# Kernel optimization log

Measured on AMD Instinct MI355X. Metric: run time of the kernel, lower is better.

## Reference

```python
import jax, jax.numpy as jnp
import numpy as np

N = 50000      # nodes
E = 400000     # edges (before self loops)
F_IN = 128     # num_features
HID = 64       # hidden_dim
HEADS = 4
G = 64         # number of graphs in batch
NCLS = 2
NEG = 0.2      # leaky relu negative slope
BN_EPS = 1e-5


def setup_inputs() -> dict:
    key = jax.random.key(0)
    ks = jax.random.split(key, 32)
    rn = lambda k, shape, s=0.05: jax.random.normal(k, shape, jnp.float32) * s
    inp = {}
    inp["x"] = jax.random.normal(ks[0], (N, F_IN), jnp.float32)
    inp["edge_index"] = jax.random.randint(ks[1], (2, E), 0, N, dtype=jnp.int32)
    inp["batch"] = jnp.sort(jax.random.randint(ks[2], (N,), 0, G, dtype=jnp.int32))
    # layer 0 GATConv (concat=True) + pre projection
    inp["conv0_W"] = rn(ks[3], (F_IN, HEADS * HID))
    inp["conv0_att_src"] = rn(ks[4], (HEADS, HID))
    inp["conv0_att_dst"] = rn(ks[5], (HEADS, HID))
    inp["conv0_bias"] = jnp.zeros((HEADS * HID,), jnp.float32)
    inp["pre0_W"] = rn(ks[6], (HEADS * HID, HID))
    inp["pre0_b"] = jnp.zeros((HID,), jnp.float32)
    # layers 1..2 GATConv (concat=False), stacked
    inp["convs_W"] = rn(ks[7], (2, HID, HEADS * HID))
    inp["convs_att_src"] = rn(ks[8], (2, HEADS, HID))
    inp["convs_att_dst"] = rn(ks[9], (2, HEADS, HID))
    inp["convs_bias"] = jnp.zeros((2, HID), jnp.float32)
    # batch norms (eval mode: running stats)
    inp["bn_gamma"] = jnp.ones((3, HID), jnp.float32)
    inp["bn_beta"] = jnp.zeros((3, HID), jnp.float32)
    inp["bn_mean"] = rn(ks[10], (3, HID), 0.1)
    inp["bn_var"] = jax.random.uniform(ks[11], (3, HID), jnp.float32) + 0.5
    # JK projection, attention pooling, classifier
    inp["jump_W"] = rn(ks[12], (3 * HID, HID))
    inp["jump_b"] = jnp.zeros((HID,), jnp.float32)
    inp["att_W"] = rn(ks[13], (HID, 1))
    inp["att_b"] = jnp.zeros((1,), jnp.float32)
    inp["cls_W1"] = rn(ks[14], (HID, HID // 2))
    inp["cls_b1"] = jnp.zeros((HID // 2,), jnp.float32)
    inp["cls_W2"] = rn(ks[15], (HID // 2, NCLS))
    inp["cls_b2"] = jnp.zeros((NCLS,), jnp.float32)
    return inp


def _segment_softmax(logits, seg, num_segments):
    m = jax.ops.segment_max(logits, seg, num_segments=num_segments)
    e = jnp.exp(logits - m[seg])
    s = jax.ops.segment_sum(e, seg, num_segments=num_segments)
    return e / s[seg]


def _gat_conv(x, src, dst, W, a_src, a_dst, bias, concat):
    n = x.shape[0]
    H, C = a_src.shape
    xh = (x @ W).reshape(n, H, C)                         # [N, H, C]
    as_n = jnp.einsum('nhc,hc->nh', xh, a_src)            # [N, H]
    ad_n = jnp.einsum('nhc,hc->nh', xh, a_dst)            # [N, H]
    logits = jax.nn.leaky_relu(as_n[src] + ad_n[dst], NEG)  # [E', H]
    att = _segment_softmax(logits, dst, n)                # softmax over incoming edges
    out = jax.ops.segment_sum(xh[src] * att[:, :, None], dst, num_segments=n)
    out = out.reshape(n, H * C) if concat else out.mean(axis=1)
    return out + bias


def _bn(h, g, b, m, v):
    return (h - m) * jax.lax.rsqrt(v + BN_EPS) * g + b


def reference(x, edge_index, batch, conv0_W, conv0_att_src, conv0_att_dst,
              conv0_bias, pre0_W, pre0_b, convs_W, convs_att_src, convs_att_dst,
              convs_bias, bn_gamma, bn_beta, bn_mean, bn_var, jump_W, jump_b,
              att_W, att_b, cls_W1, cls_b1, cls_W2, cls_b2):
    n = x.shape[0]
    loops = jnp.arange(n, dtype=edge_index.dtype)
    src = jnp.concatenate([edge_index[0], loops])         # add_self_loops=True
    dst = jnp.concatenate([edge_index[1], loops])
    reps = []
    # layer 0: concat heads -> pre projection -> BN -> ELU (no residual: 128 != 64)
    h = _gat_conv(x, src, dst, conv0_W, conv0_att_src, conv0_att_dst, conv0_bias, True)
    h = h @ pre0_W + pre0_b
    h = jax.nn.elu(_bn(h, bn_gamma[0], bn_beta[0], bn_mean[0], bn_var[0]))
    reps.append(h)
    # layers 1..2: mean heads -> BN -> ELU -> residual
    for i in range(2):
        h_in = h
        h = _gat_conv(h, src, dst, convs_W[i], convs_att_src[i], convs_att_dst[i],
                      convs_bias[i], False)
        h = jax.nn.elu(_bn(h, bn_gamma[i + 1], bn_beta[i + 1], bn_mean[i + 1], bn_var[i + 1]))
        h = h + h_in
        reps.append(h)
    # jumping knowledge (cat)
    h = jnp.concatenate(reps, axis=-1) @ jump_W + jump_b  # [N, HID]
    # attentional global pooling
    a = _segment_softmax((h @ att_W + att_b)[:, 0], batch, G)  # [N]
    hg = jax.ops.segment_sum(h * a[:, None], batch, num_segments=G)  # [G, HID]
    # classifier
    return jax.nn.relu(hg @ cls_W1 + cls_b1) @ cls_W2 + cls_b2
```

## Files before the change

kernel.cpp:

```cpp
#include <hip/hip_runtime.h>
#include <hip/hip_bf16.h>
#include <math.h>

#define NEG 0.2f
#define BNEPS 1e-5f
#define NGRAPH 64
#define SCAN_CHUNK 2048
#define POOL_BLOCKS 256

typedef short bf16x8 __attribute__((ext_vector_type(8)));
typedef float f32x4  __attribute__((ext_vector_type(4)));
typedef float f32x2  __attribute__((ext_vector_type(2)));

__device__ __forceinline__ float bf2f(unsigned short u) {
    return __uint_as_float(((unsigned)u) << 16);
}
__device__ __forceinline__ short f2bf(float f) {
    return (short)__bfloat16_as_ushort(__float2bfloat16(f));
}
__device__ __forceinline__ unsigned char f2fp8(float f) {
    int pk = __builtin_amdgcn_cvt_pk_fp8_f32(f, f, 0, false);
    return (unsigned char)(pk & 0xFF);
}

__global__ __launch_bounds__(256)
void init_kernel(const int* __restrict__ batch, int N,
                 int* __restrict__ counts, int* __restrict__ gstart,
                 float* __restrict__ hg_acc, float* __restrict__ wsum_acc)
{
    int idx = blockIdx.x * 256 + threadIdx.x;
    for (int i = idx; i < N; i += gridDim.x * 256) counts[i] = 0;
    if (blockIdx.x == 0) {
        int t = threadIdx.x;
        for (int i = t; i < NGRAPH * 64; i += 256) hg_acc[i] = 0.f;
        if (t < NGRAPH) wsum_acc[t] = 0.f;
        if (t <= NGRAPH) {
            int lo = 0, hi = N;
            while (lo < hi) {
                int mid = (lo + hi) >> 1;
                if (batch[mid] < t) lo = mid + 1; else hi = mid;
            }
            gstart[t] = lo;
        }
    }
}

__global__ __launch_bounds__(256)
void gemm_xh_mfma(const float* __restrict__ A, int lda,
                  const float* __restrict__ W, int Nc, int M, int K,
                  const float* __restrict__ att_s, const float* __restrict__ att_d,
                  float* __restrict__ as_out, float* __restrict__ ad_out,
                  unsigned char* __restrict__ C8)
{
    __shared__ short Wt[64 * 136];
    const int KP = K + 8;
    int tid  = threadIdx.x;
    int lane = tid & 63, wave = tid >> 6;
    int row0 = blockIdx.x * 64;
    int colb = blockIdx.y * 64;
    int c15 = lane & 15, q = lane >> 4;

    {
        int n = tid & 63;
        for (int k = tid >> 6; k < K; k += 4)
            Wt[n * KP + k] = f2bf(W[(size_t)k * Nc + colb + n]);
    }
    __syncthreads();

    int row = row0 + wave * 16 + c15;
    bool rok = row < M;
    const float* arow = A + (size_t)row * lda + q * 8;

    f32x4 acc[4];
    #pragma unroll
    for (int st = 0; st < 4; ++st) acc[st] = (f32x4){0.f, 0.f, 0.f, 0.f};

    for (int k0 = 0; k0 < K; k0 += 32) {
        bf16x8 av;
        if (rok) {
            float4 a0 = *(const float4*)(arow + k0);
            float4 a1 = *(const float4*)(arow + k0 + 4);
            av[0] = f2bf(a0.x); av[1] = f2bf(a0.y); av[2] = f2bf(a0.z); av[3] = f2bf(a0.w);
            av[4] = f2bf(a1.x); av[5] = f2bf(a1.y); av[6] = f2bf(a1.z); av[7] = f2bf(a1.w);
        } else {
            av = (bf16x8){0,0,0,0,0,0,0,0};
        }
        #pragma unroll
        for (int st = 0; st < 4; ++st) {
            bf16x8 bv = *(const bf16x8*)(Wt + (st * 16 + c15) * KP + k0 + q * 8);
            acc[st] = __builtin_amdgcn_mfma_f32_16x16x32_bf16(av, bv, acc[st], 0, 0, 0);
        }
    }

    #pragma unroll
    for (int r = 0; r < 4; ++r) {
        int orow = row0 + wave * 16 + q * 4 + r;
        if (orow >= M) continue;
        unsigned char* cb = C8 + (size_t)orow * 256 + colb + c15;
        #pragma unroll
        for (int st = 0; st < 4; ++st)
            cb[st * 16] = f2fp8(acc[st][r]);
    }
    float sa[4], da[4];
    #pragma unroll
    for (int st = 0; st < 4; ++st) {
        sa[st] = att_s[colb + st * 16 + c15];
        da[st] = att_d[colb + st * 16 + c15];
    }
    #pragma unroll
    for (int r = 0; r < 4; ++r) {
        float ps = acc[0][r] * sa[0] + acc[1][r] * sa[1] + acc[2][r] * sa[2] + acc[3][r] * sa[3];
        float pd = acc[0][r] * da[0] + acc[1][r] * da[1] + acc[2][r] * da[2] + acc[3][r] * da[3];
        #pragma unroll
        for (int o = 1; o < 16; o <<= 1) {
            ps += __shfl_xor(ps, o);
            pd += __shfl_xor(pd, o);
        }
        int orow = row0 + wave * 16 + q * 4 + r;
        if (c15 == 0 && orow < M) {
            as_out[orow * 4 + blockIdx.y] = ps;
            ad_out[orow * 4 + blockIdx.y] = pd;
        }
    }
}

__global__ __launch_bounds__(256)
void gemm_n64_mfma(const void* __restrict__ Araw, int lda, int a_is_bf16,
                   const float* __restrict__ W, int M, int K,
                   const float* __restrict__ bias,
                   float* __restrict__ C, int ldc, int mode,
                   const float* __restrict__ bn_g, const float* __restrict__ bn_b,
                   const float* __restrict__ bn_m, const float* __restrict__ bn_v,
                   const float* __restrict__ attW, const float* __restrict__ attb,
                   float* __restrict__ wout)
{
    __shared__ short Wt[64 * 264];
    const int KP = K + 8;
    int tid  = threadIdx.x;
    int lane = tid & 63, wave = tid >> 6;
    int row0 = blockIdx.x * 64;
    int c15 = lane & 15, q = lane >> 4;

    {
        int n = tid & 63;
        for (int k = tid >> 6; k < K; k += 4)
            Wt[n * KP + k] = f2bf(W[(size_t)k * 64 + n]);
    }
    __syncthreads();

    int row = row0 + wave * 16 + c15;
    bool rok = row < M;

    f32x4 acc[4];
    #pragma unroll
    for (int st = 0; st < 4; ++st) acc[st] = (f32x4){0.f, 0.f, 0.f, 0.f};

    for (int k0 = 0; k0 < K; k0 += 32) {
        bf16x8 av;
        if (rok) {
            if (a_is_bf16) {
                av = *(const bf16x8*)((const unsigned short*)Araw
                                      + (size_t)row * lda + k0 + q * 8);
            } else {
                const float* ap = (const float*)Araw + (size_t)row * lda + k0 + q * 8;
                float4 a0 = *(const float4*)ap;
                float4 a1 = *(const float4*)(ap + 4);
                av[0] = f2bf(a0.x); av[1] = f2bf(a0.y); av[2] = f2bf(a0.z); av[3] = f2bf(a0.w);
                av[4] = f2bf(a1.x); av[5] = f2bf(a1.y); av[6] = f2bf(a1.z); av[7] = f2bf(a1.w);
            }
        } else {
            av = (bf16x8){0,0,0,0,0,0,0,0};
        }
        #pragma unroll
        for (int st = 0; st < 4; ++st) {
            bf16x8 bv = *(const bf16x8*)(Wt + (st * 16 + c15) * KP + k0 + q * 8);
            acc[st] = __builtin_amdgcn_mfma_f32_16x16x32_bf16(av, bv, acc[st], 0, 0, 0);
        }
    }

    #pragma unroll
    for (int st = 0; st < 4; ++st) {
        int col = st * 16 + c15;
        float bs = bias ? bias[col] : 0.f;
        float sg = 1.f, sb = 0.f;
        if (mode == 1) {
            sg = bn_g[col] / sqrtf(bn_v[col] + BNEPS);
            sb = bn_b[col] - bn_m[col] * sg;
        }
        #pragma unroll
        for (int r = 0; r < 4; ++r) {
            int orow = row0 + wave * 16 + q * 4 + r;
            if (orow >= M) continue;
            float v = acc[st][r] + bs;
            if (mode == 1) {
                v = v * sg + sb;
                v = v > 0.f ? v : __expf(v) - 1.f;
            }
            acc[st][r] = v;
            C[(size_t)orow * ldc + col] = v;
        }
    }

    if (wout) {
        float sa[4];
        #pragma unroll
        for (int st = 0; st < 4; ++st) sa[st] = attW[st * 16 + c15];
        float ab = attb[0];
        #pragma unroll
        for (int r = 0; r < 4; ++r) {
            float ps = acc[0][r] * sa[0] + acc[1][r] * sa[1]
                     + acc[2][r] * sa[2] + acc[3][r] * sa[3];
            #pragma unroll
            for (int o = 1; o < 16; o <<= 1) ps += __shfl_xor(ps, o);
            int orow = row0 + wave * 16 + q * 4 + r;
            if (c15 == 0 && orow < M) wout[orow] = __expf(ps + ab);
        }
    }
}

__global__ __launch_bounds__(256)
void hist_kernel(const int* __restrict__ ei, int E, int N, int* __restrict__ counts)
{
    int e = blockIdx.x * blockDim.x + threadIdx.x;
    int Etot = E + N;
    if (e >= Etot) return;
    int d = (e < E) ? ei[E + e] : e - E;
    atomicAdd(&counts[d], 1);
}

__global__ __launch_bounds__(256)
void scan_phase1(const int* __restrict__ counts, int N, int* __restrict__ blocksum)
{
    __shared__ int wsum[4];
    int tid = threadIdx.x, lane = tid & 63, wave = tid >> 6;
    int base = blockIdx.x * SCAN_CHUNK;
    int s = 0;
    #pragma unroll
    for (int j = 0; j < SCAN_CHUNK / 256; ++j) {
        int idx = base + tid + j * 256;
        if (idx < N) s += counts[idx];
    }
    #pragma unroll
    for (int o = 32; o; o >>= 1) s += __shfl_xor(s, o);
    if (lane == 0) wsum[wave] = s;
    __syncthreads();
    if (tid == 0) blocksum[blockIdx.x] = wsum[0] + wsum[1] + wsum[2] + wsum[3];
}

__global__ __launch_bounds__(256)
void scan_phase3(const int* __restrict__ counts, int N, int nb,
                 const int* __restrict__ blocksum,
                 int* __restrict__ rowptr, int* __restrict__ cursor)
{
    __shared__ int wsum[4];
    __shared__ int pref[64];
    int tid = threadIdx.x, lane = tid & 63, wave = tid >> 6;

    if (wave == 0) {
        int v = (lane < nb) ? blocksum[lane] : 0;
        int incl = v;
        #pragma unroll
        for (int o = 1; o < 64; o <<= 1) {
            int t = __shfl_up(incl, o);
            if (lane >= o) incl += t;
        }
        pref[lane] = incl;
    }
    __syncthreads();
    int boff = blockIdx.x ? pref[blockIdx.x - 1] : 0;
    if (blockIdx.x == 0 && tid == 0) rowptr[N] = pref[nb - 1];

    int start = blockIdx.x * SCAN_CHUNK + tid * 8;
    int v[8];
    int s = 0;
    #pragma unroll
    for (int j = 0; j < 8; ++j) {
        v[j] = (start + j < N) ? counts[start + j] : 0;
        s += v[j];
    }
    int incl = s;
    #pragma unroll
    for (int o = 1; o < 64; o <<= 1) {
        int t = __shfl_up(incl, o);
        if (lane >= o) incl += t;
    }
    if (lane == 63) wsum[wave] = incl;
    __syncthreads();
    int woff = 0;
    #pragma unroll
    for (int w = 0; w < 4; ++w) if (w < wave) woff += wsum[w];
    int run = boff + woff + incl - s;
    #pragma unroll
    for (int j = 0; j < 8; ++j) {
        int idx = start + j;
        if (idx < N) { rowptr[idx] = run; cursor[idx] = run; }
        run += v[j];
    }
}

__global__ __launch_bounds__(256)
void scatter_kernel(const int* __restrict__ ei, int E, int N,
                    int* __restrict__ cursor, int* __restrict__ csr_src)
{
    int e = blockIdx.x * blockDim.x + threadIdx.x;
    int Etot = E + N;
    if (e >= Etot) return;
    int s, d;
    if (e < E) { s = ei[e]; d = ei[E + e]; } else { s = d = e - E; }
    int pos = atomicAdd(&cursor[d], 1);
    csr_src[pos] = s;
}

__global__ __launch_bounds__(256)
void aggregate_kernel(const int* __restrict__ rowptr, const int* __restrict__ csr_src,
                      const float* __restrict__ as_n, const float* __restrict__ ad_n,
                      const unsigned char* __restrict__ xh8,
                      const float* __restrict__ bias,
                      float* __restrict__ outp, int ldo,
                      int N, int mode,
                      const float* __restrict__ bn_g, const float* __restrict__ bn_b,
                      const float* __restrict__ bn_m, const float* __restrict__ bn_v,
                      const float* __restrict__ resid)
{
    int node = (blockIdx.x * blockDim.x + threadIdx.x) >> 6;
    int lane = threadIdx.x & 63;
    if (node >= N) return;
    int h = lane >> 4, li = lane & 15, grp = lane & 48;
    int e0 = rowptr[node], e1 = rowptr[node + 1];
    float adh = ad_n[node * 4 + h];
    unsigned laneoff = (unsigned)(lane * 4);

    float4 acc = make_float4(0.f, 0.f, 0.f, 0.f);
    float wsum = 0.f;

    for (int base = e0; base < e1; base += 16) {
        int cnt = e1 - base; if (cnt > 16) cnt = 16;
        int s = 0; float w = 0.f;
        if (li < cnt) {
            s = csr_src[base + li];
            float l = as_n[s * 4 + h] + adh;
            l = fmaxf(l, NEG * l);
            w = __expf(l);
        }
        int k = 0;
        for (; k + 3 < cnt; k += 4) {
            float w0 = __shfl(w, grp + k),     w1 = __shfl(w, grp + k + 1);
            float w2 = __shfl(w, grp + k + 2), w3 = __shfl(w, grp + k + 3);
            int s0 = __shfl(s, grp + k),       s1 = __shfl(s, grp + k + 1);
            int s2 = __shfl(s, grp + k + 2),   s3 = __shfl(s, grp + k + 3);
            unsigned x0 = *(const unsigned*)(xh8 + ((unsigned)s0 * 256u + laneoff));
            unsigned x1 = *(const unsigned*)(xh8 + ((unsigned)s1 * 256u + laneoff));
            unsigned x2 = *(const unsigned*)(xh8 + ((unsigned)s2 * 256u + laneoff));
            unsigned x3 = *(const unsigned*)(xh8 + ((unsigned)s3 * 256u + laneoff));
            f32x2 l0 = __builtin_amdgcn_cvt_pk_f32_fp8((int)x0, false);
            f32x2 h0 = __builtin_amdgcn_cvt_pk_f32_fp8((int)x0, true);
            f32x2 l1 = __builtin_amdgcn_cvt_pk_f32_fp8((int)x1, false);
            f32x2 h1 = __builtin_amdgcn_cvt_pk_f32_fp8((int)x1, true);
            f32x2 l2 = __builtin_amdgcn_cvt_pk_f32_fp8((int)x2, false);
            f32x2 h2 = __builtin_amdgcn_cvt_pk_f32_fp8((int)x2, true);
            f32x2 l3 = __builtin_amdgcn_cvt_pk_f32_fp8((int)x3, false);
            f32x2 h3 = __builtin_amdgcn_cvt_pk_f32_fp8((int)x3, true);
            acc.x += w0 * l0.x; acc.y += w0 * l0.y; acc.z += w0 * h0.x; acc.w += w0 * h0.y;
            acc.x += w1 * l1.x; acc.y += w1 * l1.y; acc.z += w1 * h1.x; acc.w += w1 * h1.y;
            acc.x += w2 * l2.x; acc.y += w2 * l2.y; acc.z += w2 * h2.x; acc.w += w2 * h2.y;
            acc.x += w3 * l3.x; acc.y += w3 * l3.y; acc.z += w3 * h3.x; acc.w += w3 * h3.y;
            wsum += (w0 + w1) + (w2 + w3);
        }
        for (; k < cnt; ++k) {
            float wk = __shfl(w, grp + k);
            int sk = __shfl(s, grp + k);
            unsigned xv = *(const unsigned*)(xh8 + ((unsigned)sk * 256u + laneoff));
            f32x2 lo = __builtin_amdgcn_cvt_pk_f32_fp8((int)xv, false);
            f32x2 hi = __builtin_amdgcn_cvt_pk_f32_fp8((int)xv, true);
            acc.x += wk * lo.x; acc.y += wk * lo.y;
            acc.z += wk * hi.x; acc.w += wk * hi.y;
            wsum += wk;
        }
    }

    float rw = 1.f / wsum;
    acc.x *= rw; acc.y *= rw; acc.z *= rw; acc.w *= rw;

    if (mode == 0) {
        float4 bs = *(const float4*)(bias + lane * 4);
        ushort4 pk;
        pk.x = (unsigned short)f2bf(acc.x + bs.x);
        pk.y = (unsigned short)f2bf(acc.y + bs.y);
        pk.z = (unsigned short)f2bf(acc.z + bs.z);
        pk.w = (unsigned short)f2bf(acc.w + bs.w);
        *(ushort4*)((unsigned short*)outp + (size_t)node * 256 + lane * 4) = pk;
    } else {
        #pragma unroll
        for (int off = 16; off <= 32; off <<= 1) {
            acc.x += __shfl_xor(acc.x, off);
            acc.y += __shfl_xor(acc.y, off);
            acc.z += __shfl_xor(acc.z, off);
            acc.w += __shfl_xor(acc.w, off);
        }
        if (lane < 16) {
            int cin = lane * 4;
            float4 bs = *(const float4*)(bias + cin);
            float4 g = *(const float4*)(bn_g + cin);
            float4 b = *(const float4*)(bn_b + cin);
            float4 m = *(const float4*)(bn_m + cin);
            float4 vv = *(const float4*)(bn_v + cin);
            float4 rs = *(const float4*)(resid + (size_t)node * ldo + cin);
            float o[4] = {acc.x, acc.y, acc.z, acc.w};
            float bb[4] = {bs.x, bs.y, bs.z, bs.w};
            float gg[4] = {g.x, g.y, g.z, g.w};
            float be[4] = {b.x, b.y, b.z, b.w};
            float mm[4] = {m.x, m.y, m.z, m.w};
            float va[4] = {vv.x, vv.y, vv.z, vv.w};
            float rr[4] = {rs.x, rs.y, rs.z, rs.w};
            float4 res;
            float* rp = &res.x;
            #pragma unroll
            for (int j = 0; j < 4; ++j) {
                float v = 0.25f * o[j] + bb[j];
                float sg = gg[j] / sqrtf(va[j] + BNEPS);
                v = (v - mm[j]) * sg + be[j];
                v = v > 0.f ? v : __expf(v) - 1.f;
                rp[j] = v + rr[j];
            }
            *(float4*)(outp + (size_t)node * ldo + cin) = res;
        }
    }
}

__global__ __launch_bounds__(256)
void pool_partial(const float* __restrict__ hjk, const float* __restrict__ w,
                  const int* __restrict__ batch, const int* __restrict__ gstart,
                  float* __restrict__ hg_acc, float* __restrict__ wsum_acc, int N)
{
    __shared__ float red[256];
    __shared__ float wred[4];
    int tid = threadIdx.x;
    int c = tid & 63, q = tid >> 6;
    int slab = (N + POOL_BLOCKS - 1) / POOL_BLOCKS;
    int n0 = blockIdx.x * slab;
    int n1 = n0 + slab; if (n1 > N) n1 = N;
    if (n0 >= n1) return;
    int g0 = batch[n0], g1 = batch[n1 - 1];

    for (int g = g0; g <= g1; ++g) {
        int s = gstart[g];     if (s < n0) s = n0;
        int e = gstart[g + 1]; if (e > n1) e = n1;
        float acc = 0.f, ws = 0.f;
        for (int n = s + q; n < e; n += 4) {
            float wn = w[n];
            acc += wn * hjk[(size_t)n * 64 + c];
            if (c == 0) ws += wn;
        }
        red[tid] = acc;
        if (c == 0) wred[q] = ws;
        __syncthreads();
        if (q == 0) {
            float v = red[c] + red[64 + c] + red[128 + c] + red[192 + c];
            if (v != 0.f) atomicAdd(&hg_acc[g * 64 + c], v);
            if (c == 0) {
                float t = wred[0] + wred[1] + wred[2] + wred[3];
                if (t != 0.f) atomicAdd(&wsum_acc[g], t);
            }
        }
        __syncthreads();
    }
}

__global__ void cls_kernel(const float* __restrict__ hg_acc,
                           const float* __restrict__ wsum_acc,
                           const float* __restrict__ W1, const float* __restrict__ b1,
                           const float* __restrict__ W2, const float* __restrict__ b2,
                           float* __restrict__ out)
{
    int g = blockIdx.x, t = threadIdx.x;
    __shared__ float z[32];
    __shared__ float h[64];
    float wsum = wsum_acc[g];
    float rw = (wsum > 0.f) ? 1.f / wsum : 0.f;
    h[t] = hg_acc[g * 64 + t] * rw;
    h[t + 32] = hg_acc[g * 64 + t + 32] * rw;
    __syncthreads();
    float acc = b1[t];
    for (int k = 0; k < 64; ++k) acc += h[k] * W1[k * 32 + t];
    z[t] = fmaxf(acc, 0.f);
    __syncthreads();
    if (t < 2) {
        float o = b2[t];
        for (int j = 0; j < 32; ++j) o += z[j] * W2[j * 2 + t];
        out[g * 2 + t] = o;
    }
}

extern "C" void kernel_launch(void* const* d_in, const int* in_sizes, int n_in,
                              void* d_out, int out_size, void* d_ws, size_t ws_size,
                              hipStream_t stream)
{
    const float* x        = (const float*)d_in[0];
    const int*   ei       = (const int*)d_in[1];
    const int*   batch    = (const int*)d_in[2];
    const float* conv0_W  = (const float*)d_in[3];
    const float* conv0_as = (const float*)d_in[4];
    const float* conv0_ad = (const float*)d_in[5];
    const float* conv0_b  = (const float*)d_in[6];
    const float* pre0_W   = (const float*)d_in[7];
    const float* pre0_b   = (const float*)d_in[8];
    const float* convs_W  = (const float*)d_in[9];
    const float* convs_as = (const float*)d_in[10];
    const float* convs_ad = (const float*)d_in[11];
    const float* convs_b  = (const float*)d_in[12];
    const float* bn_g     = (const float*)d_in[13];
    const float* bn_b     = (const float*)d_in[14];
    const float* bn_m     = (const float*)d_in[15];
    const float* bn_v     = (const float*)d_in[16];
    const float* jump_W   = (const float*)d_in[17];
    const float* jump_b   = (const float*)d_in[18];
    const float* att_W    = (const float*)d_in[19];
    const float* att_b    = (const float*)d_in[20];
    const float* cls_W1   = (const float*)d_in[21];
    const float* cls_b1   = (const float*)d_in[22];
    const float* cls_W2   = (const float*)d_in[23];
    const float* cls_b2   = (const float*)d_in[24];
    float* out = (float*)d_out;

    const int N = in_sizes[0] / 128;
    const int E = in_sizes[1] / 2;
    const int Etot = E + N;
    const int nb = (N + SCAN_CHUNK - 1) / SCAN_CHUNK;

    float* ws      = (float*)d_ws;
    unsigned char* xh8      = (unsigned char*)ws;
    unsigned short* h256_bf = (unsigned short*)ws + (size_t)N * 256;
    float* repsAll = (float*)(h256_bf + (size_t)N * 256);
    float* as_n    = repsAll + (size_t)N * 192;
    float* ad_n    = as_n + (size_t)N * 4;
    float* hjk     = ad_n + (size_t)N * 4;
    float* hg_acc  = hjk + (size_t)N * 64;
    float* wsum_acc= hg_acc + NGRAPH * 64;
    int*   rowptr  = (int*)(wsum_acc + NGRAPH);
    int*   cursor  = rowptr + (N + 1);
    int*   counts  = cursor + N;
    int*   csr_src = counts + N;
    int*   gstart  = csr_src + Etot;
    int*   blocksum = gstart + (NGRAPH + 1);
    float* wbuf    = as_n;

    dim3 blk(256);
    int node_wave_blocks = (N + 3) / 4;
    int edge_blocks      = (Etot + 255) / 256;
    int row_blocks       = (N + 63) / 64;

    init_kernel<<<64, blk, 0, stream>>>(batch, N, counts, gstart, hg_acc, wsum_acc);
    hist_kernel<<<edge_blocks, blk, 0, stream>>>(ei, E, N, counts);
    scan_phase1<<<nb, blk, 0, stream>>>(counts, N, blocksum);
    scan_phase3<<<nb, blk, 0, stream>>>(counts, N, nb, blocksum, rowptr, cursor);
    scatter_kernel<<<edge_blocks, blk, 0, stream>>>(ei, E, N, cursor, csr_src);

    {
        dim3 g1(row_blocks, 4);
        gemm_xh_mfma<<<g1, blk, 0, stream>>>(x, 128, conv0_W, 256, N, 128,
                                             conv0_as, conv0_ad, as_n, ad_n, xh8);
        aggregate_kernel<<<node_wave_blocks, blk, 0, stream>>>(
            rowptr, csr_src, as_n, ad_n, xh8, conv0_b, (float*)h256_bf, 256, N, 0,
            nullptr, nullptr, nullptr, nullptr, nullptr);
        gemm_n64_mfma<<<row_blocks, blk, 0, stream>>>(h256_bf, 256, 1, pre0_W, N, 256,
                                                      pre0_b, repsAll, 192, 1,
                                                      bn_g, bn_b, bn_m, bn_v,
                                                      nullptr, nullptr, nullptr);
    }

    for (int i = 0; i < 2; ++i) {
        dim3 g1(row_blocks, 4);
        gemm_xh_mfma<<<g1, blk, 0, stream>>>(repsAll + i * 64, 192,
                                             convs_W + (size_t)i * 64 * 256, 256, N, 64,
                                             convs_as + i * 256, convs_ad + i * 256,
                                             as_n, ad_n, xh8);
        aggregate_kernel<<<node_wave_blocks, blk, 0, stream>>>(
            rowptr, csr_src, as_n, ad_n, xh8, convs_b + i * 64,
            repsAll + (i + 1) * 64, 192, N, 1,
            bn_g + (i + 1) * 64, bn_b + (i + 1) * 64,
            bn_m + (i + 1) * 64, bn_v + (i + 1) * 64,
            repsAll + i * 64);
    }

    gemm_n64_mfma<<<row_blocks, blk, 0, stream>>>(repsAll, 192, 0, jump_W, N, 192,
                                                  jump_b, hjk, 64, 0,
                                                  nullptr, nullptr, nullptr, nullptr,
                                                  att_W, att_b, wbuf);

    pool_partial<<<POOL_BLOCKS, blk, 0, stream>>>(hjk, wbuf, batch, gstart,
                                                  hg_acc, wsum_acc, N);
    cls_kernel<<<NGRAPH, 32, 0, stream>>>(hg_acc, wsum_acc, cls_W1, cls_b1,
                                          cls_W2, cls_b2, out);
}
```

Baseline: 373.3 us.

## Reorder GAT layers 1-2 to aggregate 64-wide inputs before projecting

```diff
diff --git a/kernel.cpp b/kernel.cpp
--- a/kernel.cpp
+++ b/kernel.cpp
@@ -26,7 +26,10 @@
 __global__ __launch_bounds__(256)
 void init_kernel(const int* __restrict__ batch, int N,
                  int* __restrict__ counts, int* __restrict__ gstart,
-                 float* __restrict__ hg_acc, float* __restrict__ wsum_acc)
+                 float* __restrict__ hg_acc, float* __restrict__ wsum_acc,
+                 const float* __restrict__ convs_W,
+                 const float* __restrict__ convs_as, const float* __restrict__ convs_ad,
+                 float* __restrict__ uv)
 {
     int idx = blockIdx.x * 256 + threadIdx.x;
     for (int i = idx; i < N; i += gridDim.x * 256) counts[i] = 0;
@@ -43,6 +46,19 @@
             gstart[t] = lo;
         }
     }
+    if (blockIdx.x == 1) {
+        int t = threadIdx.x;
+        int h = t >> 6, k = t & 63;
+        for (int i = 0; i < 2; ++i) {
+            const float* Wr  = convs_W + (size_t)i * 64 * 256 + k * 256 + h * 64;
+            const float* av  = convs_as + i * 256 + h * 64;
+            const float* dv  = convs_ad + i * 256 + h * 64;
+            float su = 0.f, sv = 0.f;
+            for (int c = 0; c < 64; ++c) { su += Wr[c] * av[c]; sv += Wr[c] * dv[c]; }
+            uv[i * 256 + h * 64 + k]       = su;
+            uv[512 + i * 256 + h * 64 + k] = sv;
+        }
+    }
 }
 
 __global__ __launch_bounds__(256)
@@ -126,11 +142,15 @@
 
 __global__ __launch_bounds__(256)
 void gemm_n64_mfma(const void* __restrict__ Araw, int lda, int a_is_bf16,
-                   const float* __restrict__ W, int M, int K,
-                   const float* __restrict__ bias,
+                   const float* __restrict__ W, int w_gat, int M, int K,
+                   const float* __restrict__ bias, float scale,
                    float* __restrict__ C, int ldc, int mode,
                    const float* __restrict__ bn_g, const float* __restrict__ bn_b,
                    const float* __restrict__ bn_m, const float* __restrict__ bn_v,
+                   const float* __restrict__ resid, int ldr,
+                   unsigned char* __restrict__ h8_out,
+                   const float* __restrict__ u, const float* __restrict__ v,
+                   float* __restrict__ as_out, float* __restrict__ ad_out,
                    const float* __restrict__ attW, const float* __restrict__ attb,
                    float* __restrict__ wout)
 {
@@ -143,8 +163,10 @@
 
     {
         int n = tid & 63;
-        for (int k = tid >> 6; k < K; k += 4)
-            Wt[n * KP + k] = f2bf(W[(size_t)k * 64 + n]);
+        for (int k = tid >> 6; k < K; k += 4) {
+            int widx = w_gat ? ((k & 63) * 256 + (k >> 6) * 64 + n) : (k * 64 + n);
+            Wt[n * KP + k] = f2bf(W[widx]);
+        }
     }
     __syncthreads();
 
@@ -191,13 +213,60 @@
         for (int r = 0; r < 4; ++r) {
             int orow = row0 + wave * 16 + q * 4 + r;
             if (orow >= M) continue;
-            float v = acc[st][r] + bs;
+            float vvv = acc[st][r] * scale + bs;
             if (mode == 1) {
-                v = v * sg + sb;
-                v = v > 0.f ? v : __expf(v) - 1.f;
-            }
-            acc[st][r] = v;
-            C[(size_t)orow * ldc + col] = v;
+                vvv = vvv * sg + sb;
+                vvv = vvv > 0.f ? vvv : __expf(vvv) - 1.f;
+            }
+            if (resid) vvv += resid[(size_t)orow * ldr + col];
+            acc[st][r] = vvv;
+            C[(size_t)orow * ldc + col] = vvv;
+        }
+    }
+
+    if (h8_out) {
+        #pragma unroll
+        for (int r = 0; r < 4; ++r) {
+            int orow = row0 + wave * 16 + q * 4 + r;
+            if (orow >= M) continue;
+            unsigned char* hb = h8_out + (size_t)orow * 64 + c15;
+            #pragma unroll
+            for (int st = 0; st < 4; ++st)
+                hb[st * 16] = f2fp8(acc[st][r]);
+        }
+    }
+
+    if (u) {
+        float uu[4][4], vv2[4][4];
+        #pragma unroll
+        for (int h = 0; h < 4; ++h)
+            #pragma unroll
+            for (int st = 0; st < 4; ++st) {
+                uu[h][st]  = u[h * 64 + st * 16 + c15];
+                vv2[h][st] = v[h * 64 + st * 16 + c15];
+            }
+        #pragma unroll
+        for (int r = 0; r < 4; ++r) {
+            int orow = row0 + wave * 16 + q * 4 + r;
+            float pv[8];
+            #pragma unroll
+            for (int h = 0; h < 4; ++h) {
+                pv[h]     = acc[0][r] * uu[h][0] + acc[1][r] * uu[h][1]
+                          + acc[2][r] * uu[h][2] + acc[3][r] * uu[h][3];
+                pv[4 + h] = acc[0][r] * vv2[h][0] + acc[1][r] * vv2[h][1]
+                          + acc[2][r] * vv2[h][2] + acc[3][r] * vv2[h][3];
+            }
+            #pragma unroll
+            for (int jj = 0; jj < 8; ++jj)
+                #pragma unroll
+                for (int o = 1; o < 16; o <<= 1) pv[jj] += __shfl_xor(pv[jj], o);
+            if (c15 == 0 && orow < M) {
+                #pragma unroll
+                for (int h = 0; h < 4; ++h) {
+                    as_out[orow * 4 + h] = pv[h];
+                    ad_out[orow * 4 + h] = pv[4 + h];
+                }
+            }
         }
     }
 
@@ -316,11 +385,7 @@
                       const float* __restrict__ as_n, const float* __restrict__ ad_n,
                       const unsigned char* __restrict__ xh8,
                       const float* __restrict__ bias,
-                      float* __restrict__ outp, int ldo,
-                      int N, int mode,
-                      const float* __restrict__ bn_g, const float* __restrict__ bn_b,
-                      const float* __restrict__ bn_m, const float* __restrict__ bn_v,
-                      const float* __restrict__ resid)
+                      unsigned short* __restrict__ outp, int N)
 {
     int node = (blockIdx.x * blockDim.x + threadIdx.x) >> 6;
     int lane = threadIdx.x & 63;
@@ -379,52 +444,81 @@
     }
 
     float rw = 1.f / wsum;
-    acc.x *= rw; acc.y *= rw; acc.z *= rw; acc.w *= rw;
-
-    if (mode == 0) {
-        float4 bs = *(const float4*)(bias + lane * 4);
-        ushort4 pk;
-        pk.x = (unsigned short)f2bf(acc.x + bs.x);
-        pk.y = (unsigned short)f2bf(acc.y + bs.y);
-        pk.z = (unsigned short)f2bf(acc.z + bs.z);
-        pk.w = (unsigned short)f2bf(acc.w + bs.w);
-        *(ushort4*)((unsigned short*)outp + (size_t)node * 256 + lane * 4) = pk;
-    } else {
-        #pragma unroll
-        for (int off = 16; off <= 32; off <<= 1) {
-            acc.x += __shfl_xor(acc.x, off);
-            acc.y += __shfl_xor(acc.y, off);
-            acc.z += __shfl_xor(acc.z, off);
-            acc.w += __shfl_xor(acc.w, off);
-        }
-        if (lane < 16) {
-            int cin = lane * 4;
-            float4 bs = *(const float4*)(bias + cin);
-            float4 g = *(const float4*)(bn_g + cin);
-            float4 b = *(const float4*)(bn_b + cin);
-            float4 m = *(const float4*)(bn_m + cin);
-            float4 vv = *(const float4*)(bn_v + cin);
-            float4 rs = *(const float4*)(resid + (size_t)node * ldo + cin);
-            float o[4] = {acc.x, acc.y, acc.z, acc.w};
-            float bb[4] = {bs.x, bs.y, bs.z, bs.w};
-            float gg[4] = {g.x, g.y, g.z, g.w};
-            float be[4] = {b.x, b.y, b.z, b.w};
-            float mm[4] = {m.x, m.y, m.z, m.w};
-            float va[4] = {vv.x, vv.y, vv.z, vv.w};
-            float rr[4] = {rs.x, rs.y, rs.z, rs.w};
-            float4 res;
-            float* rp = &res.x;
-            #pragma unroll
-            for (int j = 0; j < 4; ++j) {
-                float v = 0.25f * o[j] + bb[j];
-                float sg = gg[j] / sqrtf(va[j] + BNEPS);
-                v = (v - mm[j]) * sg + be[j];
-                v = v > 0.f ? v : __expf(v) - 1.f;
-                rp[j] = v + rr[j];
-            }
-            *(float4*)(outp + (size_t)node * ldo + cin) = res;
-        }
-    }
+    float4 bs = *(const float4*)(bias + lane * 4);
+    ushort4 pk;
+    pk.x = (unsigned short)f2bf(acc.x * rw + bs.x);
+    pk.y = (unsigned short)f2bf(acc.y * rw + bs.y);
+    pk.z = (unsigned short)f2bf(acc.z * rw + bs.z);
+    pk.w = (unsigned short)f2bf(acc.w * rw + bs.w);
+    *(ushort4*)(outp + (size_t)node * 256 + lane * 4) = pk;
+}
+
+__global__ __launch_bounds__(256)
+void aggregate_z(const int* __restrict__ rowptr, const int* __restrict__ csr_src,
+                 const float* __restrict__ as_n, const float* __restrict__ ad_n,
+                 const unsigned char* __restrict__ h8,
+                 unsigned short* __restrict__ zout, int N)
+{
+    int node = (blockIdx.x * blockDim.x + threadIdx.x) >> 6;
+    int lane = threadIdx.x & 63;
+    if (node >= N) return;
+    int g = lane >> 4, li = lane & 15, grp = lane & 48;
+    int e0 = rowptr[node], e1 = rowptr[node + 1];
+    float adh = ad_n[node * 4 + g];
+
+    float acc[4][4];
+    #pragma unroll
+    for (int h = 0; h < 4; ++h)
+        #pragma unroll
+        for (int j = 0; j < 4; ++j) acc[h][j] = 0.f;
+    float wsum = 0.f;
+
+    for (int base = e0; base < e1; base += 16) {
+        int cnt = e1 - base; if (cnt > 16) cnt = 16;
+        int s = 0; float w = 0.f;
+        if (li < cnt) {
+            s = csr_src[base + li];
+            float l = as_n[s * 4 + g] + adh;
+            l = fmaxf(l, NEG * l);
+            w = __expf(l);
+        }
+        wsum += w;
+        for (int k = 0; k < cnt; k += 4) {
+            int m = k + g;
+            int   sm = __shfl(s, grp + m);
+            float w0 = __shfl(w, m);
+            float w1 = __shfl(w, 16 + m);
+            float w2 = __shfl(w, 32 + m);
+            float w3 = __shfl(w, 48 + m);
+            if (m < cnt) {
+                unsigned xv = *(const unsigned*)(h8 + ((unsigned)sm * 64u + (unsigned)(li * 4)));
+                f32x2 lo = __builtin_amdgcn_cvt_pk_f32_fp8((int)xv, false);
+                f32x2 hi = __builtin_amdgcn_cvt_pk_f32_fp8((int)xv, true);
+                float f0 = lo.x, f1 = lo.y, f2 = hi.x, f3 = hi.y;
+                acc[0][0] += w0 * f0; acc[0][1] += w0 * f1; acc[0][2] += w0 * f2; acc[0][3] += w0 * f3;
+                acc[1][0] += w1 * f0; acc[1][1] += w1 * f1; acc[1][2] += w1 * f2; acc[1][3] += w1 * f3;
+                acc[2][0] += w2 * f0; acc[2][1] += w2 * f1; acc[2][2] += w2 * f2; acc[2][3] += w2 * f3;
+                acc[3][0] += w3 * f0; acc[3][1] += w3 * f1; acc[3][2] += w3 * f2; acc[3][3] += w3 * f3;
+            }
+        }
+    }
+
+    #pragma unroll
+    for (int o = 1; o < 16; o <<= 1) wsum += __shfl_xor(wsum, o);
+    #pragma unroll
+    for (int h = 0; h < 4; ++h)
+        #pragma unroll
+        for (int j = 0; j < 4; ++j) {
+            acc[h][j] += __shfl_xor(acc[h][j], 16);
+            acc[h][j] += __shfl_xor(acc[h][j], 32);
+        }
+    float rw = 1.f / wsum;
+    ushort4 pk;
+    pk.x = (unsigned short)f2bf(acc[g][0] * rw);
+    pk.y = (unsigned short)f2bf(acc[g][1] * rw);
+    pk.z = (unsigned short)f2bf(acc[g][2] * rw);
+    pk.w = (unsigned short)f2bf(acc[g][3] * rw);
+    *(ushort4*)(zout + (size_t)node * 256 + g * 64 + li * 4) = pk;
 }
 
 __global__ __launch_bounds__(256)
@@ -542,6 +636,8 @@
     int*   csr_src = counts + N;
     int*   gstart  = csr_src + Etot;
     int*   blocksum = gstart + (NGRAPH + 1);
+    float* uv      = (float*)(blocksum + 64);
+    unsigned char* h8 = xh8;
     float* wbuf    = as_n;
 
     dim3 blk(256);
@@ -549,7 +645,8 @@
     int edge_blocks      = (Etot + 255) / 256;
     int row_blocks       = (N + 63) / 64;
 
-    init_kernel<<<64, blk, 0, stream>>>(batch, N, counts, gstart, hg_acc, wsum_acc);
+    init_kernel<<<64, blk, 0, stream>>>(batch, N, counts, gstart, hg_acc, wsum_acc,
+                                        convs_W, convs_as, convs_ad, uv);
     hist_kernel<<<edge_blocks, blk, 0, stream>>>(ei, E, N, counts);
     scan_phase1<<<nb, blk, 0, stream>>>(counts, N, blocksum);
     scan_phase3<<<nb, blk, 0, stream>>>(counts, N, nb, blocksum, rowptr, cursor);
@@ -560,32 +657,35 @@
         gemm_xh_mfma<<<g1, blk, 0, stream>>>(x, 128, conv0_W, 256, N, 128,
                                              conv0_as, conv0_ad, as_n, ad_n, xh8);
         aggregate_kernel<<<node_wave_blocks, blk, 0, stream>>>(
-            rowptr, csr_src, as_n, ad_n, xh8, conv0_b, (float*)h256_bf, 256, N, 0,
-            nullptr, nullptr, nullptr, nullptr, nullptr);
-        gemm_n64_mfma<<<row_blocks, blk, 0, stream>>>(h256_bf, 256, 1, pre0_W, N, 256,
-                                                      pre0_b, repsAll, 192, 1,
-                                                      bn_g, bn_b, bn_m, bn_v,
-                                                      nullptr, nullptr, nullptr);
-    }
-
-    for (int i = 0; i < 2; ++i) {
-        dim3 g1(row_blocks, 4);
-        gemm_xh_mfma<<<g1, blk, 0, stream>>>(repsAll + i * 64, 192,
-                                             convs_W + (size_t)i * 64 * 256, 256, N, 64,
-                                             convs_as + i * 256, convs_ad + i * 256,
-                                             as_n, ad_n, xh8);
-        aggregate_kernel<<<node_wave_blocks, blk, 0, stream>>>(
-            rowptr, csr_src, as_n, ad_n, xh8, convs_b + i * 64,
-            repsAll + (i + 1) * 64, 192, N, 1,
-            bn_g + (i + 1) * 64, bn_b + (i + 1) * 64,
-            bn_m + (i + 1) * 64, bn_v + (i + 1) * 64,
-            repsAll + i * 64);
-    }
-
-    gemm_n64_mfma<<<row_blocks, blk, 0, stream>>>(repsAll, 192, 0, jump_W, N, 192,
-                                                  jump_b, hjk, 64, 0,
-                                                  nullptr, nullptr, nullptr, nullptr,
-                                                  att_W, att_b, wbuf);
+            rowptr, csr_src, as_n, ad_n, xh8, conv0_b, h256_bf, N);
+        gemm_n64_mfma<<<row_blocks, blk, 0, stream>>>(
+            h256_bf, 256, 1, pre0_W, 0, N, 256, pre0_b, 1.f,
+            repsAll, 192, 1, bn_g, bn_b, bn_m, bn_v,
+            nullptr, 0, h8, uv, uv + 512, as_n, ad_n,
+            nullptr, nullptr, nullptr);
+    }
+
+    aggregate_z<<<node_wave_blocks, blk, 0, stream>>>(rowptr, csr_src, as_n, ad_n,
+                                                      h8, h256_bf, N);
+    gemm_n64_mfma<<<row_blocks, blk, 0, stream>>>(
+        h256_bf, 256, 1, convs_W, 1, N, 256, convs_b, 0.25f,
+        repsAll + 64, 192, 1, bn_g + 64, bn_b + 64, bn_m + 64, bn_v + 64,
+        repsAll, 192, h8, uv + 256, uv + 512 + 256, as_n, ad_n,
+        nullptr, nullptr, nullptr);
+
+    aggregate_z<<<node_wave_blocks, blk, 0, stream>>>(rowptr, csr_src, as_n, ad_n,
+                                                      h8, h256_bf, N);
+    gemm_n64_mfma<<<row_blocks, blk, 0, stream>>>(
+        h256_bf, 256, 1, convs_W + (size_t)64 * 256, 1, N, 256, convs_b + 64, 0.25f,
+        repsAll + 128, 192, 1, bn_g + 128, bn_b + 128, bn_m + 128, bn_v + 128,
+        repsAll + 64, 192, nullptr, nullptr, nullptr, nullptr, nullptr,
+        nullptr, nullptr, nullptr);
+
+    gemm_n64_mfma<<<row_blocks, blk, 0, stream>>>(
+        repsAll, 192, 0, jump_W, 0, N, 192, jump_b, 1.f,
+        hjk, 64, 0, nullptr, nullptr, nullptr, nullptr,
+        nullptr, 0, nullptr, nullptr, nullptr, nullptr, nullptr,
+        att_W, att_b, wbuf);
 
     pool_partial<<<POOL_BLOCKS, blk, 0, stream>>>(hjk, wbuf, batch, gstart,
                                                   hg_acc, wsum_acc, N);
```

New measurement: 394.5 us. +5.7%, slower.
